# Optimization experiments

Hardware: AMD Instinct MI355X
Metric: run time of the kernel (lower is better)

The kernel has to match this reference:

```python
import jax, jax.numpy as jnp
import numpy as np

H, D, VD = 8, 64, 64
QD, KD, VDIM, OUT = 512, 512, 512, 512
N, QS, VS = 16, 512, 512
TEMP = 10.0              # softstair_temp
SCALING = D ** -0.5


def _softstair(x):
    fl = jnp.floor(x)
    return fl + jax.nn.sigmoid(TEMP * (jnp.abs(x - fl) - 0.5))


def setup_inputs() -> dict:
    key = jax.random.key(0)
    ks = jax.random.split(key, 24)
    f = jax.random.normal
    s = 0.03  # xavier-ish scale
    return {
        "Q": f(ks[0], (N, QS, QD), jnp.float32),
        "K": f(ks[1], (N, VS, KD), jnp.float32),
        "V": f(ks[2], (N, VS, VDIM), jnp.float32),
        "past_state": f(ks[3], (N, H, QS, D), jnp.float32),
        "past_attention": jax.random.uniform(ks[4], (N, H, QS, 1), jnp.float32),
        "value_positions": jnp.arange(VS, dtype=jnp.float32),
        "attention_mask": jnp.ones((N, QS, VS), jnp.int32),
        "Wq": f(ks[5], (QD, H * D), jnp.float32) * s,
        "Wk": f(ks[6], (KD, H * D), jnp.float32) * s,
        "Wv": f(ks[7], (VDIM, H * VD), jnp.float32) * s,
        "Wpos": f(ks[8], (QD, H * D), jnp.float32) * s,
        "bpos": f(ks[9], (H * D,), jnp.float32) * s,
        "Wsigma": f(ks[10], (H, D, 1), jnp.float32) * s,
        "Wrho": f(ks[11], (H, D, 3), jnp.float32) * s,
        "mix_w": f(ks[12], (QD, 1), jnp.float32) * s,
        "mix_b": f(ks[13], (1,), jnp.float32) * s,
        "gru_wi": f(ks[14], (D, 3 * D), jnp.float32) * s,
        "gru_wh": f(ks[15], (D, 3 * D), jnp.float32) * s,
        "gru_bi": f(ks[16], (3 * D,), jnp.float32) * s,
        "gru_bh": f(ks[17], (3 * D,), jnp.float32) * s,
        "Wc": f(ks[18], (H * VD, OUT), jnp.float32) * s,
    }


def reference(Q, K, V, past_state, past_attention, value_positions, attention_mask,
              Wq, Wk, Wv, Wpos, bpos, Wsigma, Wrho, mix_w, mix_b,
              gru_wi, gru_wh, gru_bi, gru_bh, Wc):
    n, qS, _ = Q.shape
    vS = K.shape[1]
    mask_f = attention_mask.astype(jnp.float32)          # [N,qS,vS]
    mask_b = attention_mask.astype(bool)[:, None]        # [N,1,qS,vS]
    lengths = jnp.sum(mask_f, axis=-1)                   # [N,qS]
    l_1 = jnp.maximum(1.0, lengths - 1.0)[:, None, :, None]
    step_size = 1.0 / l_1                                # [N,1,qS,1]
    nvp = value_positions[None, None, None, :] * step_size  # [N,1,qS,vS]

    # mix gate
    mix = jax.nn.sigmoid(Q @ mix_w + mix_b)[:, None]     # [N,1,qS,1]

    # projections -> [N,H,S,d]
    Qpos = (Q @ Wpos + bpos).reshape(n, qS, H, D).transpose(0, 2, 1, 3)
    Qh = (Q @ Wq).reshape(n, qS, H, D).transpose(0, 2, 1, 3)
    Kh = (K @ Wk).reshape(n, vS, H, D).transpose(0, 2, 1, 3)
    Vh = (V @ Wv).reshape(n, vS, H, VD).transpose(0, 2, 1, 3)

    # content attention
    content = jnp.einsum('bhqd,bhkd->bhqk', Qh, Kh) * SCALING
    content_attn = jax.nn.softmax(jnp.where(mask_b, content, -jnp.inf), axis=-1)

    # GRUCell update (torch gate order r,z,n) on relu(Qpos) with past_state
    x = jax.nn.relu(Qpos)
    gi = x @ gru_wi + gru_bi
    gh = past_state @ gru_wh + gru_bh
    ir, iz, inn = jnp.split(gi, 3, axis=-1)
    hr, hz, hn = jnp.split(gh, 3, axis=-1)
    r = jax.nn.sigmoid(ir + hr)
    z = jax.nn.sigmoid(iz + hz)
    nn_ = jnp.tanh(inn + r * hn)
    state = (1.0 - z) * nn_ + z * past_state             # [N,H,qS,D]

    # location (Gaussian) attention
    sigma = (jax.nn.relu(jnp.einsum('bhqd,hde->bhqe', state, Wsigma)) + 0.27) \
            / lengths[:, None, :, None]                  # [N,H,qS,1]
    rho = jnp.einsum('bhqd,hde->bhqe', state, Wrho)      # [N,H,qS,3]
    steps = _softstair(rho[..., 0:1])
    attn_gate = jax.nn.sigmoid(rho[..., 1:2])
    bias_gate = jax.nn.sigmoid(rho[..., 2:3])
    mu_ = steps * step_size + attn_gate * past_attention + bias_gate
    # leaky clamp to [0,1]
    mu = jnp.maximum(0.01 * mu_, jnp.minimum(mu_, 1.0 + 0.01 * mu_))
    diff = nvp - mu                                      # [N,H,qS,vS]
    gauss = jnp.exp(-(diff * diff) / (2.0 * sigma * sigma))
    g = gauss * mask_f[:, None]
    pos_attn = g / jnp.sum(g + 1e-20, axis=-1, keepdims=True)

    scores = mix * pos_attn + (1.0 - mix) * content_attn
    attended = jnp.einsum('bhqk,bhkv->bhqv', scores, Vh)
    out = attended.transpose(0, 2, 1, 3).reshape(n, qS, H * VD) @ Wc
    return out
```

## Files before the change

### kernel.cpp

```cpp
#include <hip/hip_runtime.h>


typedef __bf16 bf16;
typedef __bf16 bfx8 __attribute__((ext_vector_type(8)));
typedef float v4f __attribute__((ext_vector_type(4)));

__device__ inline float sigm(float x) { return 1.0f / (1.0f + expf(-x)); }

__device__ inline v4f mfma16(bfx8 a, bfx8 b, v4f c) {
    return __builtin_amdgcn_mfma_f32_16x16x32_bf16(a, b, c, 0, 0, 0);
}

__device__ inline void split8(const float* __restrict__ p, bfx8& hi, bfx8& lo) {
    float4 x = *(const float4*)p;
    float4 y = *(const float4*)(p + 4);
    float v[8] = {x.x, x.y, x.z, x.w, y.x, y.y, y.z, y.w};
#pragma unroll
    for (int j = 0; j < 8; ++j) {
        bf16 h = (bf16)v[j];
        hi[j] = h;
        lo[j] = (bf16)(v[j] - (float)h);
    }
}

__device__ inline unsigned short bfbits(float v) {
    bf16 h = (bf16)v;
    return __builtin_bit_cast(unsigned short, h);
}
__device__ inline float bffrom(unsigned short u) {
    return (float)__builtin_bit_cast(bf16, u);
}

__global__ __launch_bounds__(256) void conv_qkv_kernel(
    const float* __restrict__ s0, const float* __restrict__ s1, const float* __restrict__ s2,
    bf16* __restrict__ d0, bf16* __restrict__ d1, bf16* __restrict__ d2) {
    int tb = blockIdx.x >> 11;
    const float* src = tb == 0 ? s0 : (tb == 1 ? s1 : s2);
    bf16* dst = tb == 0 ? d0 : (tb == 1 ? d1 : d2);
    long i0 = (long)(blockIdx.x & 2047) * 2048 + threadIdx.x * 8;
    float4 x = *(const float4*)(src + i0);
    float4 y = *(const float4*)(src + i0 + 4);
    bfx8 o;
    o[0] = (bf16)x.x; o[1] = (bf16)x.y; o[2] = (bf16)x.z; o[3] = (bf16)x.w;
    o[4] = (bf16)y.x; o[5] = (bf16)y.y; o[6] = (bf16)y.z; o[7] = (bf16)y.w;
    *(bfx8*)(dst + i0) = o;
}

struct TW { const float* src[5]; bf16* dst[5]; bf16* dstlo[5]; };

__global__ __launch_bounds__(256) void trans_w_kernel(TW a) {
    __shared__ float tile[64][68];
    const float* src = a.src[blockIdx.y];
    bf16* dst = a.dst[blockIdx.y];
    bf16* dlo = a.dstlo[blockIdx.y];
    const int rbase = (blockIdx.x >> 3) * 64, cbase = (blockIdx.x & 7) * 64;
    const int t = threadIdx.x;
    const int r = t >> 2, cc = (t & 3) * 16;
    {
        const float* p = src + (long)(rbase + r) * 512 + cbase + cc;
        float4 x0 = *(const float4*)p, x1 = *(const float4*)(p + 4);
        float4 x2 = *(const float4*)(p + 8), x3 = *(const float4*)(p + 12);
        *(float4*)(&tile[r][cc]) = x0;
        *(float4*)(&tile[r][cc + 4]) = x1;
        *(float4*)(&tile[r][cc + 8]) = x2;
        *(float4*)(&tile[r][cc + 12]) = x3;
    }
    __syncthreads();
    {
        bfx8 h0, h1, l0, l1;
#pragma unroll
        for (int j = 0; j < 8; ++j) {
            float v0 = tile[cc + j][r];
            float v1 = tile[cc + 8 + j][r];
            bf16 a0 = (bf16)v0, a1 = (bf16)v1;
            h0[j] = a0; l0[j] = (bf16)(v0 - (float)a0);
            h1[j] = a1; l1[j] = (bf16)(v1 - (float)a1);
        }
        bf16* p = dst + (long)(cbase + r) * 512 + rbase + cc;
        *(bfx8*)p = h0;
        *(bfx8*)(p + 8) = h1;
        if (dlo) {
            bf16* pl = dlo + (long)(cbase + r) * 512 + rbase + cc;
            *(bfx8*)pl = l0;
            *(bfx8*)(pl + 8) = l1;
        }
    }
}

__global__ void gru_prep_kernel(const float* __restrict__ gwi, const float* __restrict__ gwh,
                                bf16* ih, bf16* il, bf16* hh, bf16* hl) {
    const float* src = blockIdx.x ? gwh : gwi;
    bf16* dh = blockIdx.x ? hh : ih;
    bf16* dl = blockIdx.x ? hl : il;
    int n = threadIdx.x;
    for (int k = 0; k < 64; ++k) {
        float v = src[k * 192 + n];
        bf16 h = (bf16)v;
        dh[n * 64 + k] = h;
        dl[n * 64 + k] = (bf16)(v - (float)h);
    }
}

template <bool TRANSC, typename OutT>
__global__ __launch_bounds__(256) void gemm_bt(
    const bf16* __restrict__ A, const bf16* __restrict__ BT,
    OutT* __restrict__ C) {
    __shared__ bf16 As[64][72];
    __shared__ bf16 Bs[64][72];

    const int mbase = blockIdx.x * 64, nbase = blockIdx.y * 64;
    const int t = threadIdx.x;
    const int wave = t >> 6, lane = t & 63;
    const int quad = lane >> 4, c = lane & 15;
    const int wrow = (wave >> 1) * 32, wcol = (wave & 1) * 32;

    const v4f zero4 = {0.f, 0.f, 0.f, 0.f};
    v4f acc[2][2];
    acc[0][0] = zero4; acc[0][1] = zero4; acc[1][0] = zero4; acc[1][1] = zero4;

    const int sr = t >> 2, sch = t & 3;

    for (int k0 = 0; k0 < 512; k0 += 32) {
        bfx8 va = *(const bfx8*)(A + (long)(mbase + sr) * 512 + k0 + sch * 8);
        bfx8 vb = *(const bfx8*)(BT + (long)(nbase + sr) * 512 + k0 + sch * 8);
        *(bfx8*)(&As[sr][sch * 8]) = va;
        *(bfx8*)(&Bs[sr][sch * 8]) = vb;
        __syncthreads();

        bfx8 a0 = *(const bfx8*)(&As[wrow + c][quad * 8]);
        bfx8 a1 = *(const bfx8*)(&As[wrow + 16 + c][quad * 8]);
        bfx8 b0 = *(const bfx8*)(&Bs[wcol + c][quad * 8]);
        bfx8 b1 = *(const bfx8*)(&Bs[wcol + 16 + c][quad * 8]);
        acc[0][0] = mfma16(a0, b0, acc[0][0]);
        acc[0][1] = mfma16(a0, b1, acc[0][1]);
        acc[1][0] = mfma16(a1, b0, acc[1][0]);
        acc[1][1] = mfma16(a1, b1, acc[1][1]);
        __syncthreads();
    }

    if (TRANSC) {
#pragma unroll
        for (int tm = 0; tm < 2; ++tm)
#pragma unroll
            for (int tn = 0; tn < 2; ++tn)
#pragma unroll
                for (int i = 0; i < 4; ++i) {
                    int rl = wrow + tm * 16 + quad * 4 + i;
                    int cl = wcol + tn * 16 + c;
                    As[cl][rl] = (bf16)acc[tm][tn][i];
                }
        __syncthreads();
        OutT* CT = C + ((long)(mbase >> 9)) * 262144 + (long)nbase * 512 + (mbase & 511);
        const int rr = t >> 2, kc = (t & 3) * 16;
        bfx8 o0, o1;
#pragma unroll
        for (int j = 0; j < 8; ++j) { o0[j] = As[rr][kc + j]; o1[j] = As[rr][kc + 8 + j]; }
        *(bfx8*)(CT + (long)rr * 512 + kc) = o0;
        *(bfx8*)(CT + (long)rr * 512 + kc + 8) = o1;
    } else {
#pragma unroll
        for (int tm = 0; tm < 2; ++tm)
#pragma unroll
            for (int tn = 0; tn < 2; ++tn)
#pragma unroll
                for (int i = 0; i < 4; ++i) {
                    int row = mbase + wrow + tm * 16 + quad * 4 + i;
                    int col = nbase + wcol + tn * 16 + c;
                    C[(long)row * 512 + col] = (OutT)acc[tm][tn][i];
                }
    }
}

__global__ __launch_bounds__(256) void gemm_split_hl(
    const float* __restrict__ A, const bf16* __restrict__ BTh,
    const bf16* __restrict__ BTl, const float* __restrict__ bias,
    bf16* __restrict__ Ch, bf16* __restrict__ Cl) {
    __shared__ bf16 Ah[64][72], Al[64][72];
    __shared__ bf16 Bh[64][72], Bl[64][72];

    const int mbase = blockIdx.x * 64, nbase = blockIdx.y * 64;
    const int t = threadIdx.x;
    const int wave = t >> 6, lane = t & 63;
    const int quad = lane >> 4, c = lane & 15;
    const int wrow = (wave >> 1) * 32, wcol = (wave & 1) * 32;

    const v4f zero4 = {0.f, 0.f, 0.f, 0.f};
    v4f acc[2][2];
    acc[0][0] = zero4; acc[0][1] = zero4; acc[1][0] = zero4; acc[1][1] = zero4;

    const int sr = t >> 2, sch = t & 3;

    for (int k0 = 0; k0 < 512; k0 += 32) {
        bfx8 h, l;
        split8(A + (long)(mbase + sr) * 512 + k0 + sch * 8, h, l);
        *(bfx8*)(&Ah[sr][sch * 8]) = h;
        *(bfx8*)(&Al[sr][sch * 8]) = l;
        *(bfx8*)(&Bh[sr][sch * 8]) = *(const bfx8*)(BTh + (long)(nbase + sr) * 512 + k0 + sch * 8);
        *(bfx8*)(&Bl[sr][sch * 8]) = *(const bfx8*)(BTl + (long)(nbase + sr) * 512 + k0 + sch * 8);
        __syncthreads();

        bfx8 ah0 = *(const bfx8*)(&Ah[wrow + c][quad * 8]);
        bfx8 ah1 = *(const bfx8*)(&Ah[wrow + 16 + c][quad * 8]);
        bfx8 al0 = *(const bfx8*)(&Al[wrow + c][quad * 8]);
        bfx8 al1 = *(const bfx8*)(&Al[wrow + 16 + c][quad * 8]);
        bfx8 bh0 = *(const bfx8*)(&Bh[wcol + c][quad * 8]);
        bfx8 bh1 = *(const bfx8*)(&Bh[wcol + 16 + c][quad * 8]);
        bfx8 bl0 = *(const bfx8*)(&Bl[wcol + c][quad * 8]);
        bfx8 bl1 = *(const bfx8*)(&Bl[wcol + 16 + c][quad * 8]);
        acc[0][0] = mfma16(ah0, bh0, acc[0][0]);
        acc[0][0] = mfma16(ah0, bl0, acc[0][0]);
        acc[0][0] = mfma16(al0, bh0, acc[0][0]);
        acc[0][1] = mfma16(ah0, bh1, acc[0][1]);
        acc[0][1] = mfma16(ah0, bl1, acc[0][1]);
        acc[0][1] = mfma16(al0, bh1, acc[0][1]);
        acc[1][0] = mfma16(ah1, bh0, acc[1][0]);
        acc[1][0] = mfma16(ah1, bl0, acc[1][0]);
        acc[1][0] = mfma16(al1, bh0, acc[1][0]);
        acc[1][1] = mfma16(ah1, bh1, acc[1][1]);
        acc[1][1] = mfma16(ah1, bl1, acc[1][1]);
        acc[1][1] = mfma16(al1, bh1, acc[1][1]);
        __syncthreads();
    }

#pragma unroll
    for (int tm = 0; tm < 2; ++tm)
#pragma unroll
        for (int tn = 0; tn < 2; ++tn)
#pragma unroll
            for (int i = 0; i < 4; ++i) {
                int row = mbase + wrow + tm * 16 + quad * 4 + i;
                int col = nbase + wcol + tn * 16 + c;
                float v = fmaxf(acc[tm][tn][i] + bias[col], 0.f);
                bf16 h = (bf16)v;
                Ch[(long)row * 512 + col] = h;
                Cl[(long)row * 512 + col] = (bf16)(v - (float)h);
            }
}

__global__ __launch_bounds__(256) void mix_len_kernel(
    const float* __restrict__ Q, const int* __restrict__ mask,
    const float* __restrict__ mix_w, const float* __restrict__ mix_b,
    float* __restrict__ mixv, float* __restrict__ stepv, float* __restrict__ lenv,
    unsigned* __restrict__ maskbits) {
    int row = blockIdx.x * 4 + (threadIdx.x >> 6);
    int lane = threadIdx.x & 63;
    float dot = 0.f, ms = 0.f;
    unsigned myw = 0;
#pragma unroll
    for (int j = 0; j < 8; ++j) {
        float qv = Q[(long)row * 512 + j * 64 + lane];
        float wv = mix_w[j * 64 + lane];
        dot += qv * wv;
        int mv = mask[(long)row * 512 + j * 64 + lane];
        unsigned long long b = __ballot(mv != 0);
        ms += (float)__popcll(b);
        if ((lane >> 1) == j) myw = (unsigned)(b >> ((lane & 1) * 32));
    }
#pragma unroll
    for (int o = 32; o > 0; o >>= 1) dot += __shfl_xor(dot, o);
    if (lane < 16) maskbits[(long)row * 16 + lane] = myw;
    if (lane == 0) {
        mixv[row] = sigm(dot + mix_b[0]);
        lenv[row] = ms;
        stepv[row] = 1.0f / fmaxf(1.0f, ms - 1.0f);
    }
}

__global__ __launch_bounds__(256) void gru_fused_kernel(
    const bf16* __restrict__ Xh, const bf16* __restrict__ Xl,
    const float* __restrict__ hp,
    const bf16* __restrict__ wih, const bf16* __restrict__ wil,
    const bf16* __restrict__ whh, const bf16* __restrict__ whl,
    const float* __restrict__ gbi, const float* __restrict__ gbh,
    const float* __restrict__ pa, const float* __restrict__ Wsigma,
    const float* __restrict__ Wrho,
    const float* __restrict__ lenv, const float* __restrict__ stepv,
    float* __restrict__ muv, float* __restrict__ sigv) {
    __shared__ bf16 Wh[192][72], Wl[192][72];
    __shared__ float biL[384];

    const int b = blockIdx.x;
    const int qb = b & 7, nh = b >> 3, hd = nh & 7, n = nh >> 3;
    const int t = threadIdx.x;
    const int w = t >> 6, lane = t & 63, quad = lane >> 4, c = lane & 15;
    const int q0 = qb * 64 + w * 16;

    if (t < 192) { biL[t] = gbi[t]; biL[192 + t] = gbh[t]; }
#pragma unroll
    for (int it = 0; it < 6; ++it) {
        int task = it * 256 + t;
        int r = task >> 3, ch = task & 7;
        *(bfx8*)(&Wh[r][ch * 8]) = *(const bfx8*)(wih + r * 64 + ch * 8);
        *(bfx8*)(&Wl[r][ch * 8]) = *(const bfx8*)(wil + r * 64 + ch * 8);
    }
    __syncthreads();

    const v4f zero4 = {0.f, 0.f, 0.f, 0.f};
    v4f gi[12], gh[12];
#pragma unroll
    for (int nt = 0; nt < 12; ++nt) gi[nt] = zero4;
#pragma unroll
    for (int ks = 0; ks < 2; ++ks) {
        long ao = (long)(n * 512 + q0 + c) * 512 + hd * 64 + ks * 32 + quad * 8;
        bfx8 xh = *(const bfx8*)(Xh + ao);
        bfx8 xl = *(const bfx8*)(Xl + ao);
#pragma unroll
        for (int nt = 0; nt < 12; ++nt) {
            bfx8 bh = *(const bfx8*)(&Wh[nt * 16 + c][ks * 32 + quad * 8]);
            bfx8 bl = *(const bfx8*)(&Wl[nt * 16 + c][ks * 32 + quad * 8]);
            gi[nt] = mfma16(xh, bh, gi[nt]);
            gi[nt] = mfma16(xh, bl, gi[nt]);
            gi[nt] = mfma16(xl, bh, gi[nt]);
        }
    }
    __syncthreads();
#pragma unroll
    for (int it = 0; it < 6; ++it) {
        int task = it * 256 + t;
        int r = task >> 3, ch = task & 7;
        *(bfx8*)(&Wh[r][ch * 8]) = *(const bfx8*)(whh + r * 64 + ch * 8);
        *(bfx8*)(&Wl[r][ch * 8]) = *(const bfx8*)(whl + r * 64 + ch * 8);
    }
    __syncthreads();
#pragma unroll
    for (int nt = 0; nt < 12; ++nt) gh[nt] = zero4;
#pragma unroll
    for (int ks = 0; ks < 2; ++ks) {
        bfx8 ah, al;
        split8(hp + (long)(nh * 512 + q0 + c) * 64 + ks * 32 + quad * 8, ah, al);
#pragma unroll
        for (int nt = 0; nt < 12; ++nt) {
            bfx8 bh = *(const bfx8*)(&Wh[nt * 16 + c][ks * 32 + quad * 8]);
            bfx8 bl = *(const bfx8*)(&Wl[nt * 16 + c][ks * 32 + quad * 8]);
            gh[nt] = mfma16(ah, bh, gh[nt]);
            gh[nt] = mfma16(ah, bl, gh[nt]);
            gh[nt] = mfma16(al, bh, gh[nt]);
        }
    }

    float st[4][4];
#pragma unroll
    for (int t4 = 0; t4 < 4; ++t4) {
        float bir = biL[t4 * 16 + c];
        float biz = biL[64 + t4 * 16 + c];
        float bin = biL[128 + t4 * 16 + c];
        float bhr = biL[192 + t4 * 16 + c];
        float bhz = biL[256 + t4 * 16 + c];
        float bhn = biL[320 + t4 * 16 + c];
#pragma unroll
        for (int i = 0; i < 4; ++i) {
            int row = q0 + quad * 4 + i;
            float r = sigm(gi[t4][i] + bir + gh[t4][i] + bhr);
            float z = sigm(gi[t4 + 4][i] + biz + gh[t4 + 4][i] + bhz);
            float nn_ = tanhf(gi[t4 + 8][i] + bin + r * (gh[t4 + 8][i] + bhn));
            float hpv = hp[(long)(nh * 512 + row) * 64 + t4 * 16 + c];
            st[t4][i] = (1.0f - z) * nn_ + z * hpv;
        }
    }

    float ws_[4], wr0[4], wr1[4], wr2[4];
#pragma unroll
    for (int t4 = 0; t4 < 4; ++t4) {
        int d = t4 * 16 + c;
        ws_[t4] = Wsigma[hd * 64 + d];
        wr0[t4] = Wrho[(hd * 64 + d) * 3 + 0];
        wr1[t4] = Wrho[(hd * 64 + d) * 3 + 1];
        wr2[t4] = Wrho[(hd * 64 + d) * 3 + 2];
    }
#pragma unroll
    for (int i = 0; i < 4; ++i) {
        float s0 = 0.f, s1 = 0.f, s2 = 0.f, s3 = 0.f;
#pragma unroll
        for (int t4 = 0; t4 < 4; ++t4) {
            float sv = st[t4][i];
            s0 += sv * ws_[t4];
            s1 += sv * wr0[t4];
            s2 += sv * wr1[t4];
            s3 += sv * wr2[t4];
        }
#pragma unroll
        for (int o = 1; o < 16; o <<= 1) {
            s0 += __shfl_xor(s0, o);
            s1 += __shfl_xor(s1, o);
            s2 += __shfl_xor(s2, o);
            s3 += __shfl_xor(s3, o);
        }
        if (c == 0) {
            int row = q0 + quad * 4 + i;
            int idx = nh * 512 + row, rq = n * 512 + row;
            float L = lenv[rq], sp = stepv[rq];
            float sg = (fmaxf(s0, 0.f) + 0.27f) / L;
            float fl = floorf(s1);
            float steps = fl + sigm(10.0f * (fabsf(s1 - fl) - 0.5f));
            float ag = sigm(s2), bg = sigm(s3);
            float mu_ = steps * sp + ag * pa[idx] + bg;
            float mu = fmaxf(0.01f * mu_, fminf(mu_, 1.0f + 0.01f * mu_));
            muv[idx] = mu;
            sigv[idx] = sg;
        }
    }
}

__global__ __launch_bounds__(256) void attn_fused_kernel(
    const bf16* __restrict__ Qh, const bf16* __restrict__ Kh,
    const bf16* __restrict__ VhT, const unsigned* __restrict__ maskbits,
    const float* __restrict__ vpos, const float* __restrict__ mixv,
    const float* __restrict__ stepv, const float* __restrict__ muv,
    const float* __restrict__ sigv, bf16* __restrict__ att) {
    __shared__ alignas(16) char KVraw[128 * 72 * 2];
    __shared__ bf16 Qs[16][72];
    __shared__ bf16 Plds[16][520];
    __shared__ float vps[512];
    __shared__ float rmax[4][16], rsum[4][16], rgsum[4][16];
    __shared__ float rowmu[16], rowsig[16], rowstep[16], rowmix[16];
    bf16 (*Ks)[72] = (bf16(*)[72])KVraw;
    bf16 (*Vs)[136] = (bf16(*)[136])KVraw;

    const int b = blockIdx.x;
    const int qt = b & 31, nh = b >> 5, hd = nh & 7, n = nh >> 3;
    const int t = threadIdx.x;

    if (t < 16) {
        int q = qt * 16 + t;
        int idx = nh * 512 + q, rq = n * 512 + q;
        rowmu[t] = muv[idx];
        rowsig[t] = sigv[idx];
        rowstep[t] = stepv[rq];
        rowmix[t] = mixv[rq];
    }
    vps[t] = vpos[t];
    vps[256 + t] = vpos[256 + t];
    if (t < 128) {
        int r = t >> 3, ch = t & 7;
        bfx8 v = *(const bfx8*)(Qh + (long)(n * 512 + qt * 16 + r) * 512 + hd * 64 + ch * 8);
        *(bfx8*)(&Qs[r][ch * 8]) = v;
    }
    __syncthreads();

    const int wave = t >> 6, lane = t & 63;
    const int quad = lane >> 4, c = lane & 15;
    const int qloc = quad * 4;

    bfx8 afr0 = *(const bfx8*)(&Qs[c][quad * 8]);
    bfx8 afr1 = *(const bfx8*)(&Qs[c][32 + quad * 8]);

    const v4f zero4 = {0.f, 0.f, 0.f, 0.f};
    v4f acc[8];
#pragma unroll
    for (int i = 0; i < 8; ++i) acc[i] = zero4;

#pragma unroll
    for (int ph = 0; ph < 4; ++ph) {
#pragma unroll
        for (int it = 0; it < 4; ++it) {
            int task = it * 256 + t;
            int r = task >> 3, ch = task & 7;
            *(bfx8*)(&Ks[r][ch * 8]) =
                *(const bfx8*)(Kh + (long)(n * 512 + ph * 128 + r) * 512 + hd * 64 + ch * 8);
        }
        __syncthreads();
#pragma unroll
        for (int tt = 0; tt < 2; ++tt) {
            int t8 = ph * 2 + tt;
            int kr = wave * 32 + tt * 16 + c;
            bfx8 b0 = *(const bfx8*)(&Ks[kr][quad * 8]);
            bfx8 b1 = *(const bfx8*)(&Ks[kr][32 + quad * 8]);
            acc[t8] = mfma16(afr0, b0, acc[t8]);
            acc[t8] = mfma16(afr1, b1, acc[t8]);
        }
        __syncthreads();
    }

#pragma unroll
    for (int t8 = 0; t8 < 8; ++t8) acc[t8] = acc[t8] * 0.125f;

    unsigned mw[4][4];
#pragma unroll
    for (int i = 0; i < 4; ++i) {
        const unsigned* mrow = maskbits + (long)(n * 512 + qt * 16 + qloc + i) * 16 + wave;
        mw[i][0] = mrow[0];
        mw[i][1] = mrow[4];
        mw[i][2] = mrow[8];
        mw[i][3] = mrow[12];
    }

#pragma unroll
    for (int i = 0; i < 4; ++i) {
        float mx = -3.0e38f;
#pragma unroll
        for (int t8 = 0; t8 < 8; ++t8)
            if ((mw[i][t8 >> 1] >> ((t8 & 1) * 16 + c)) & 1) mx = fmaxf(mx, acc[t8][i]);
        mx = fmaxf(mx, __shfl_xor(mx, 1));
        mx = fmaxf(mx, __shfl_xor(mx, 2));
        mx = fmaxf(mx, __shfl_xor(mx, 4));
        mx = fmaxf(mx, __shfl_xor(mx, 8));
        if (c == 0) rmax[wave][qloc + i] = mx;
    }
    __syncthreads();

    float gmx[4], inv2s[4];
#pragma unroll
    for (int i = 0; i < 4; ++i) {
        gmx[i] = fmaxf(fmaxf(rmax[0][qloc + i], rmax[1][qloc + i]),
                       fmaxf(rmax[2][qloc + i], rmax[3][qloc + i]));
        float sg = rowsig[qloc + i];
        inv2s[i] = 0.5f / (sg * sg);
    }

    float psum[4] = {0.f, 0.f, 0.f, 0.f};
    float gsum[4] = {0.f, 0.f, 0.f, 0.f};
    unsigned pg[8][4];
#pragma unroll
    for (int t8 = 0; t8 < 8; ++t8) {
        int k = (t8 >> 1) * 128 + wave * 32 + (t8 & 1) * 16 + c;
        float vp = vps[k];
#pragma unroll
        for (int i = 0; i < 4; ++i) {
            int on = (mw[i][t8 >> 1] >> ((t8 & 1) * 16 + c)) & 1;
            float pv = on ? expf(acc[t8][i] - gmx[i]) : 0.f;
            float d = vp * rowstep[qloc + i] - rowmu[qloc + i];
            float gv = on ? expf(-(d * d) * inv2s[i]) : 0.f;
            psum[i] += pv;
            gsum[i] += gv;
            pg[t8][i] = ((unsigned)bfbits(gv) << 16) | (unsigned)bfbits(pv);
        }
    }
#pragma unroll
    for (int i = 0; i < 4; ++i) {
#pragma unroll
        for (int o = 1; o < 16; o <<= 1) {
            psum[i] += __shfl_xor(psum[i], o);
            gsum[i] += __shfl_xor(gsum[i], o);
        }
        if (c == 0) {
            rsum[wave][qloc + i] = psum[i];
            rgsum[wave][qloc + i] = gsum[i];
        }
    }
    __syncthreads();

    float ac[4], bc[4];
#pragma unroll
    for (int i = 0; i < 4; ++i) {
        float Sp = rsum[0][qloc + i] + rsum[1][qloc + i] + rsum[2][qloc + i] + rsum[3][qloc + i];
        float Sg = rgsum[0][qloc + i] + rgsum[1][qloc + i] + rgsum[2][qloc + i] +
                   rgsum[3][qloc + i] + 512.0f * 1e-20f;
        float m_ = rowmix[qloc + i];
        ac[i] = (1.0f - m_) / Sp;
        bc[i] = m_ / Sg;
    }

#pragma unroll
    for (int t8 = 0; t8 < 8; ++t8) {
        int k = (t8 >> 1) * 128 + wave * 32 + (t8 & 1) * 16 + c;
#pragma unroll
        for (int i = 0; i < 4; ++i) {
            float pv = bffrom((unsigned short)(pg[t8][i] & 0xffffu));
            float gv = bffrom((unsigned short)(pg[t8][i] >> 16));
            Plds[qloc + i][k] = (bf16)(pv * ac[i] + gv * bc[i]);
        }
    }
    __syncthreads();

    v4f accO = zero4;
#pragma unroll
    for (int ph = 0; ph < 4; ++ph) {
#pragma unroll
        for (int it = 0; it < 4; ++it) {
            int task = it * 256 + t;
            int v = task >> 4, ch = task & 15;
            *(bfx8*)(&Vs[v][ch * 8]) =
                *(const bfx8*)(VhT + (long)(n * 512 + hd * 64 + v) * 512 + ph * 128 + ch * 8);
        }
        __syncthreads();
#pragma unroll
        for (int ks = 0; ks < 4; ++ks) {
            bfx8 af = *(const bfx8*)(&Plds[c][ph * 128 + ks * 32 + quad * 8]);
            bfx8 bf_ = *(const bfx8*)(&Vs[wave * 16 + c][ks * 32 + quad * 8]);
            accO = mfma16(af, bf_, accO);
        }
        __syncthreads();
    }

#pragma unroll
    for (int i = 0; i < 4; ++i) {
        att[(long)(n * 512 + qt * 16 + quad * 4 + i) * 512 + hd * 64 + wave * 16 + c] =
            (bf16)accO[i];
    }
}

extern "C" void kernel_launch(void* const* d_in, const int* in_sizes, int n_in,
                              void* d_out, int out_size, void* d_ws, size_t ws_size,
                              hipStream_t stream) {
    (void)in_sizes; (void)n_in; (void)out_size; (void)ws_size;

    const float* Q = (const float*)d_in[0];
    const float* K = (const float*)d_in[1];
    const float* V = (const float*)d_in[2];
    const float* past_state = (const float*)d_in[3];
    const float* past_att = (const float*)d_in[4];
    const float* vpos = (const float*)d_in[5];
    const int* mask = (const int*)d_in[6];
    const float* Wq = (const float*)d_in[7];
    const float* Wk = (const float*)d_in[8];
    const float* Wv = (const float*)d_in[9];
    const float* Wpos = (const float*)d_in[10];
    const float* bpos = (const float*)d_in[11];
    const float* Wsigma = (const float*)d_in[12];
    const float* Wrho = (const float*)d_in[13];
    const float* mix_w = (const float*)d_in[14];
    const float* mix_b = (const float*)d_in[15];
    const float* gwi = (const float*)d_in[16];
    const float* gwh = (const float*)d_in[17];
    const float* gbi = (const float*)d_in[18];
    const float* gbh = (const float*)d_in[19];
    const float* Wc = (const float*)d_in[20];
    float* out = (float*)d_out;

    char* p = (char*)d_ws;
    const size_t SZB = 8192UL * 512 * 2;
    const size_t SZW = 512UL * 512 * 2;
    bf16* Qc = (bf16*)p;    p += SZB;
    bf16* Kc = (bf16*)p;    p += SZB;
    bf16* Vc = (bf16*)p;    p += SZB;
    bf16* WqT = (bf16*)p;   p += SZW;
    bf16* WkT = (bf16*)p;   p += SZW;
    bf16* WvT = (bf16*)p;   p += SZW;
    bf16* WpT = (bf16*)p;   p += SZW;
    bf16* WpTl = (bf16*)p;  p += SZW;
    bf16* WcT = (bf16*)p;   p += SZW;
    bf16* wih = (bf16*)p;   p += 24576;
    bf16* wil = (bf16*)p;   p += 24576;
    bf16* whh = (bf16*)p;   p += 24576;
    bf16* whl = (bf16*)p;   p += 24576;
    bf16* Qh = (bf16*)p;    p += SZB;
    bf16* Kh = (bf16*)p;    p += SZB;
    bf16* VhT = (bf16*)p;   p += SZB;
    bf16* Xh = (bf16*)p;
    bf16* att = Xh;         p += SZB;
    bf16* Xl = (bf16*)p;    p += SZB;
    unsigned* maskbits = (unsigned*)p;   p += 8192UL * 16 * 4;
    float* mixv = (float*)p;  p += 32768;
    float* stepv = (float*)p; p += 32768;
    float* lenv = (float*)p;  p += 32768;
    float* muv = (float*)p;   p += 262144;
    float* sigv = (float*)p;  p += 262144;

    dim3 blk(256);
    dim3 gProj(128, 8, 1);

    conv_qkv_kernel<<<dim3(6144), blk, 0, stream>>>(Q, K, V, Qc, Kc, Vc);

    TW tw;
    tw.src[0] = Wq; tw.src[1] = Wk; tw.src[2] = Wv; tw.src[3] = Wpos; tw.src[4] = Wc;
    tw.dst[0] = WqT; tw.dst[1] = WkT; tw.dst[2] = WvT; tw.dst[3] = WpT; tw.dst[4] = WcT;
    tw.dstlo[0] = nullptr; tw.dstlo[1] = nullptr; tw.dstlo[2] = nullptr;
    tw.dstlo[3] = WpTl; tw.dstlo[4] = nullptr;
    trans_w_kernel<<<dim3(64, 5), blk, 0, stream>>>(tw);

    gru_prep_kernel<<<dim3(2), dim3(192), 0, stream>>>(gwi, gwh, wih, wil, whh, whl);

    gemm_bt<false, bf16><<<gProj, blk, 0, stream>>>(Qc, WqT, Qh);
    gemm_bt<false, bf16><<<gProj, blk, 0, stream>>>(Kc, WkT, Kh);
    gemm_bt<true, bf16><<<gProj, blk, 0, stream>>>(Vc, WvT, VhT);
    gemm_split_hl<<<gProj, blk, 0, stream>>>(Q, WpT, WpTl, bpos, Xh, Xl);

    mix_len_kernel<<<dim3(2048), blk, 0, stream>>>(Q, mask, mix_w, mix_b, mixv, stepv, lenv, maskbits);

    gru_fused_kernel<<<dim3(1024), blk, 0, stream>>>(
        Xh, Xl, past_state, wih, wil, whh, whl, gbi, gbh, past_att, Wsigma, Wrho,
        lenv, stepv, muv, sigv);

    attn_fused_kernel<<<dim3(4096), blk, 0, stream>>>(
        Qh, Kh, VhT, maskbits, vpos, mixv, stepv, muv, sigv, att);

    gemm_bt<false, float><<<gProj, blk, 0, stream>>>(att, WcT, out);
}
```

Baseline: 385.2 us.

## Load attention operands directly from global, recompute exps, batch QKV GEMMs

The attention kernel no longer stages Q, K and V through shared memory. MFMA fragments are read straight from global memory, which removes the per-phase barriers, and the key ordering per wave is changed to match. Mask bits are staged once in shared memory and repacked per thread. The packed bf16 P/G values are no longer kept in registers and the exponentials are recomputed with fast __expf, trading extra math for lower register pressure. The three projection GEMMs are merged into one launch over blockIdx.z. The direct global reads rely on L2/cache reuse across waves, and __expf may lose a little precision.

```diff
diff --git a/kernel.cpp b/kernel.cpp
--- a/kernel.cpp
+++ b/kernel.cpp
@@ -5,7 +5,7 @@
 typedef __bf16 bfx8 __attribute__((ext_vector_type(8)));
 typedef float v4f __attribute__((ext_vector_type(4)));
 
-__device__ inline float sigm(float x) { return 1.0f / (1.0f + expf(-x)); }
+__device__ inline float sigm(float x) { return 1.0f / (1.0f + __expf(-x)); }
 
 __device__ inline v4f mfma16(bfx8 a, bfx8 b, v4f c) {
     return __builtin_amdgcn_mfma_f32_16x16x32_bf16(a, b, c, 0, 0, 0);
@@ -21,14 +21,6 @@
         hi[j] = h;
         lo[j] = (bf16)(v[j] - (float)h);
     }
-}
-
-__device__ inline unsigned short bfbits(float v) {
-    bf16 h = (bf16)v;
-    return __builtin_bit_cast(unsigned short, h);
-}
-__device__ inline float bffrom(unsigned short u) {
-    return (float)__builtin_bit_cast(bf16, u);
 }
 
 __global__ __launch_bounds__(256) void conv_qkv_kernel(
@@ -58,12 +50,10 @@
     const int r = t >> 2, cc = (t & 3) * 16;
     {
         const float* p = src + (long)(rbase + r) * 512 + cbase + cc;
-        float4 x0 = *(const float4*)p, x1 = *(const float4*)(p + 4);
-        float4 x2 = *(const float4*)(p + 8), x3 = *(const float4*)(p + 12);
-        *(float4*)(&tile[r][cc]) = x0;
-        *(float4*)(&tile[r][cc + 4]) = x1;
-        *(float4*)(&tile[r][cc + 8]) = x2;
-        *(float4*)(&tile[r][cc + 12]) = x3;
+        *(float4*)(&tile[r][cc]) = *(const float4*)p;
+        *(float4*)(&tile[r][cc + 4]) = *(const float4*)(p + 4);
+        *(float4*)(&tile[r][cc + 8]) = *(const float4*)(p + 8);
+        *(float4*)(&tile[r][cc + 12]) = *(const float4*)(p + 12);
     }
     __syncthreads();
     {
@@ -101,12 +91,16 @@
     }
 }
 
-template <bool TRANSC, typename OutT>
-__global__ __launch_bounds__(256) void gemm_bt(
-    const bf16* __restrict__ A, const bf16* __restrict__ BT,
-    OutT* __restrict__ C) {
+struct G3 { const bf16* A[3]; const bf16* BT[3]; bf16* C[3]; };
+
+__global__ __launch_bounds__(256) void gemm_bt3(G3 g) {
     __shared__ bf16 As[64][72];
     __shared__ bf16 Bs[64][72];
+
+    const int z = blockIdx.z;
+    const bf16* __restrict__ A = g.A[z];
+    const bf16* __restrict__ BT = g.BT[z];
+    bf16* __restrict__ C = g.C[z];
 
     const int mbase = blockIdx.x * 64, nbase = blockIdx.y * 64;
     const int t = threadIdx.x;
@@ -138,7 +132,7 @@
         __syncthreads();
     }
 
-    if (TRANSC) {
+    if (z == 2) {
 #pragma unroll
         for (int tm = 0; tm < 2; ++tm)
 #pragma unroll
@@ -150,7 +144,7 @@
                     As[cl][rl] = (bf16)acc[tm][tn][i];
                 }
         __syncthreads();
-        OutT* CT = C + ((long)(mbase >> 9)) * 262144 + (long)nbase * 512 + (mbase & 511);
+        bf16* CT = C + ((long)(mbase >> 9)) * 262144 + (long)nbase * 512 + (mbase & 511);
         const int rr = t >> 2, kc = (t & 3) * 16;
         bfx8 o0, o1;
 #pragma unroll
@@ -166,9 +160,56 @@
                 for (int i = 0; i < 4; ++i) {
                     int row = mbase + wrow + tm * 16 + quad * 4 + i;
                     int col = nbase + wcol + tn * 16 + c;
-                    C[(long)row * 512 + col] = (OutT)acc[tm][tn][i];
+                    C[(long)row * 512 + col] = (bf16)acc[tm][tn][i];
                 }
     }
+}
+
+__global__ __launch_bounds__(256) void gemm_out(
+    const bf16* __restrict__ A, const bf16* __restrict__ BT, float* __restrict__ C) {
+    __shared__ bf16 As[64][72];
+    __shared__ bf16 Bs[64][72];
+
+    const int mbase = blockIdx.x * 64, nbase = blockIdx.y * 64;
+    const int t = threadIdx.x;
+    const int wave = t >> 6, lane = t & 63;
+    const int quad = lane >> 4, c = lane & 15;
+    const int wrow = (wave >> 1) * 32, wcol = (wave & 1) * 32;
+
+    const v4f zero4 = {0.f, 0.f, 0.f, 0.f};
+    v4f acc[2][2];
+    acc[0][0] = zero4; acc[0][1] = zero4; acc[1][0] = zero4; acc[1][1] = zero4;
+
+    const int sr = t >> 2, sch = t & 3;
+
+    for (int k0 = 0; k0 < 512; k0 += 32) {
+        bfx8 va = *(const bfx8*)(A + (long)(mbase + sr) * 512 + k0 + sch * 8);
+        bfx8 vb = *(const bfx8*)(BT + (long)(nbase + sr) * 512 + k0 + sch * 8);
+        *(bfx8*)(&As[sr][sch * 8]) = va;
+        *(bfx8*)(&Bs[sr][sch * 8]) = vb;
+        __syncthreads();
+
+        bfx8 a0 = *(const bfx8*)(&As[wrow + c][quad * 8]);
+        bfx8 a1 = *(const bfx8*)(&As[wrow + 16 + c][quad * 8]);
+        bfx8 b0 = *(const bfx8*)(&Bs[wcol + c][quad * 8]);
+        bfx8 b1 = *(const bfx8*)(&Bs[wcol + 16 + c][quad * 8]);
+        acc[0][0] = mfma16(a0, b0, acc[0][0]);
+        acc[0][1] = mfma16(a0, b1, acc[0][1]);
+        acc[1][0] = mfma16(a1, b0, acc[1][0]);
+        acc[1][1] = mfma16(a1, b1, acc[1][1]);
+        __syncthreads();
+    }
+
+#pragma unroll
+    for (int tm = 0; tm < 2; ++tm)
+#pragma unroll
+        for (int tn = 0; tn < 2; ++tn)
+#pragma unroll
+            for (int i = 0; i < 4; ++i) {
+                int row = mbase + wrow + tm * 16 + quad * 4 + i;
+                int col = nbase + wcol + tn * 16 + c;
+                C[(long)row * 512 + col] = acc[tm][tn][i];
+            }
 }
 
 __global__ __launch_bounds__(256) void gemm_split_hl(
@@ -407,14 +448,11 @@
     const float* __restrict__ vpos, const float* __restrict__ mixv,
     const float* __restrict__ stepv, const float* __restrict__ muv,
     const float* __restrict__ sigv, bf16* __restrict__ att) {
-    __shared__ alignas(16) char KVraw[128 * 72 * 2];
-    __shared__ bf16 Qs[16][72];
     __shared__ bf16 Plds[16][520];
     __shared__ float vps[512];
+    __shared__ unsigned mb[16][16];
     __shared__ float rmax[4][16], rsum[4][16], rgsum[4][16];
     __shared__ float rowmu[16], rowsig[16], rowstep[16], rowmix[16];
-    bf16 (*Ks)[72] = (bf16(*)[72])KVraw;
-    bf16 (*Vs)[136] = (bf16(*)[136])KVraw;
 
     const int b = blockIdx.x;
     const int qt = b & 31, nh = b >> 5, hd = nh & 7, n = nh >> 3;
@@ -430,58 +468,42 @@
     }
     vps[t] = vpos[t];
     vps[256 + t] = vpos[256 + t];
-    if (t < 128) {
-        int r = t >> 3, ch = t & 7;
-        bfx8 v = *(const bfx8*)(Qh + (long)(n * 512 + qt * 16 + r) * 512 + hd * 64 + ch * 8);
-        *(bfx8*)(&Qs[r][ch * 8]) = v;
-    }
-    __syncthreads();
+    mb[t >> 4][t & 15] = maskbits[(long)(n * 512 + qt * 16 + (t >> 4)) * 16 + (t & 15)];
 
     const int wave = t >> 6, lane = t & 63;
     const int quad = lane >> 4, c = lane & 15;
     const int qloc = quad * 4;
 
-    bfx8 afr0 = *(const bfx8*)(&Qs[c][quad * 8]);
-    bfx8 afr1 = *(const bfx8*)(&Qs[c][32 + quad * 8]);
+    const bf16* qrow = Qh + (long)(n * 512 + qt * 16 + c) * 512 + hd * 64 + quad * 8;
+    bfx8 afr0 = *(const bfx8*)qrow;
+    bfx8 afr1 = *(const bfx8*)(qrow + 32);
 
     const v4f zero4 = {0.f, 0.f, 0.f, 0.f};
     v4f acc[8];
 #pragma unroll
     for (int i = 0; i < 8; ++i) acc[i] = zero4;
 
-#pragma unroll
-    for (int ph = 0; ph < 4; ++ph) {
-#pragma unroll
-        for (int it = 0; it < 4; ++it) {
-            int task = it * 256 + t;
-            int r = task >> 3, ch = task & 7;
-            *(bfx8*)(&Ks[r][ch * 8]) =
-                *(const bfx8*)(Kh + (long)(n * 512 + ph * 128 + r) * 512 + hd * 64 + ch * 8);
-        }
-        __syncthreads();
-#pragma unroll
-        for (int tt = 0; tt < 2; ++tt) {
-            int t8 = ph * 2 + tt;
-            int kr = wave * 32 + tt * 16 + c;
-            bfx8 b0 = *(const bfx8*)(&Ks[kr][quad * 8]);
-            bfx8 b1 = *(const bfx8*)(&Ks[kr][32 + quad * 8]);
-            acc[t8] = mfma16(afr0, b0, acc[t8]);
-            acc[t8] = mfma16(afr1, b1, acc[t8]);
-        }
-        __syncthreads();
-    }
-
+    const bf16* kbase = Kh + (long)(n * 512 + wave * 128 + c) * 512 + hd * 64 + quad * 8;
+#pragma unroll
+    for (int t8 = 0; t8 < 8; ++t8) {
+        bfx8 b0 = *(const bfx8*)(kbase + (long)t8 * 16 * 512);
+        bfx8 b1 = *(const bfx8*)(kbase + (long)t8 * 16 * 512 + 32);
+        acc[t8] = mfma16(afr0, b0, acc[t8]);
+        acc[t8] = mfma16(afr1, b1, acc[t8]);
+    }
 #pragma unroll
     for (int t8 = 0; t8 < 8; ++t8) acc[t8] = acc[t8] * 0.125f;
 
-    unsigned mw[4][4];
-#pragma unroll
-    for (int i = 0; i < 4; ++i) {
-        const unsigned* mrow = maskbits + (long)(n * 512 + qt * 16 + qloc + i) * 16 + wave;
-        mw[i][0] = mrow[0];
-        mw[i][1] = mrow[4];
-        mw[i][2] = mrow[8];
-        mw[i][3] = mrow[12];
+    __syncthreads();
+
+    unsigned mbits[4] = {0u, 0u, 0u, 0u};
+#pragma unroll
+    for (int t8 = 0; t8 < 8; ++t8) {
+        int wd = wave * 4 + (t8 >> 1);
+        int bit = (t8 & 1) * 16 + c;
+#pragma unroll
+        for (int i = 0; i < 4; ++i)
+            mbits[i] |= ((mb[qloc + i][wd] >> bit) & 1u) << t8;
     }
 
 #pragma unroll
@@ -489,7 +511,7 @@
         float mx = -3.0e38f;
 #pragma unroll
         for (int t8 = 0; t8 < 8; ++t8)
-            if ((mw[i][t8 >> 1] >> ((t8 & 1) * 16 + c)) & 1) mx = fmaxf(mx, acc[t8][i]);
+            if ((mbits[i] >> t8) & 1u) mx = fmaxf(mx, acc[t8][i]);
         mx = fmaxf(mx, __shfl_xor(mx, 1));
         mx = fmaxf(mx, __shfl_xor(mx, 2));
         mx = fmaxf(mx, __shfl_xor(mx, 4));
@@ -509,20 +531,18 @@
 
     float psum[4] = {0.f, 0.f, 0.f, 0.f};
     float gsum[4] = {0.f, 0.f, 0.f, 0.f};
-    unsigned pg[8][4];
 #pragma unroll
     for (int t8 = 0; t8 < 8; ++t8) {
-        int k = (t8 >> 1) * 128 + wave * 32 + (t8 & 1) * 16 + c;
+        int k = wave * 128 + t8 * 16 + c;
         float vp = vps[k];
 #pragma unroll
         for (int i = 0; i < 4; ++i) {
-            int on = (mw[i][t8 >> 1] >> ((t8 & 1) * 16 + c)) & 1;
-            float pv = on ? expf(acc[t8][i] - gmx[i]) : 0.f;
+            int on = (mbits[i] >> t8) & 1;
+            float pv = on ? __expf(acc[t8][i] - gmx[i]) : 0.f;
             float d = vp * rowstep[qloc + i] - rowmu[qloc + i];
-            float gv = on ? expf(-(d * d) * inv2s[i]) : 0.f;
+            float gv = on ? __expf(-(d * d) * inv2s[i]) : 0.f;
             psum[i] += pv;
             gsum[i] += gv;
-            pg[t8][i] = ((unsigned)bfbits(gv) << 16) | (unsigned)bfbits(pv);
         }
     }
 #pragma unroll
@@ -552,34 +572,26 @@
 
 #pragma unroll
     for (int t8 = 0; t8 < 8; ++t8) {
-        int k = (t8 >> 1) * 128 + wave * 32 + (t8 & 1) * 16 + c;
+        int k = wave * 128 + t8 * 16 + c;
+        float vp = vps[k];
 #pragma unroll
         for (int i = 0; i < 4; ++i) {
-            float pv = bffrom((unsigned short)(pg[t8][i] & 0xffffu));
-            float gv = bffrom((unsigned short)(pg[t8][i] >> 16));
+            int on = (mbits[i] >> t8) & 1;
+            float pv = on ? __expf(acc[t8][i] - gmx[i]) : 0.f;
+            float d = vp * rowstep[qloc + i] - rowmu[qloc + i];
+            float gv = on ? __expf(-(d * d) * inv2s[i]) : 0.f;
             Plds[qloc + i][k] = (bf16)(pv * ac[i] + gv * bc[i]);
         }
     }
     __syncthreads();
 
     v4f accO = zero4;
-#pragma unroll
-    for (int ph = 0; ph < 4; ++ph) {
-#pragma unroll
-        for (int it = 0; it < 4; ++it) {
-            int task = it * 256 + t;
-            int v = task >> 4, ch = task & 15;
-            *(bfx8*)(&Vs[v][ch * 8]) =
-                *(const bfx8*)(VhT + (long)(n * 512 + hd * 64 + v) * 512 + ph * 128 + ch * 8);
-        }
-        __syncthreads();
-#pragma unroll
-        for (int ks = 0; ks < 4; ++ks) {
-            bfx8 af = *(const bfx8*)(&Plds[c][ph * 128 + ks * 32 + quad * 8]);
-            bfx8 bf_ = *(const bfx8*)(&Vs[wave * 16 + c][ks * 32 + quad * 8]);
-            accO = mfma16(af, bf_, accO);
-        }
-        __syncthreads();
+    const bf16* vrow = VhT + (long)(n * 512 + hd * 64 + wave * 16 + c) * 512 + quad * 8;
+#pragma unroll
+    for (int ks = 0; ks < 16; ++ks) {
+        bfx8 af = *(const bfx8*)(&Plds[c][ks * 32 + quad * 8]);
+        bfx8 bf_ = *(const bfx8*)(vrow + ks * 32);
+        accO = mfma16(af, bf_, accO);
     }
 
 #pragma unroll
@@ -660,9 +672,12 @@
 
     gru_prep_kernel<<<dim3(2), dim3(192), 0, stream>>>(gwi, gwh, wih, wil, whh, whl);
 
-    gemm_bt<false, bf16><<<gProj, blk, 0, stream>>>(Qc, WqT, Qh);
-    gemm_bt<false, bf16><<<gProj, blk, 0, stream>>>(Kc, WkT, Kh);
-    gemm_bt<true, bf16><<<gProj, blk, 0, stream>>>(Vc, WvT, VhT);
+    G3 g;
+    g.A[0] = Qc; g.A[1] = Kc; g.A[2] = Vc;
+    g.BT[0] = WqT; g.BT[1] = WkT; g.BT[2] = WvT;
+    g.C[0] = Qh; g.C[1] = Kh; g.C[2] = VhT;
+    gemm_bt3<<<dim3(128, 8, 3), blk, 0, stream>>>(g);
+
     gemm_split_hl<<<gProj, blk, 0, stream>>>(Q, WpT, WpTl, bpos, Xh, Xl);
 
     mix_len_kernel<<<dim3(2048), blk, 0, stream>>>(Q, mask, mix_w, mix_b, mixv, stepv, lenv, maskbits);
@@ -674,5 +689,5 @@
     attn_fused_kernel<<<dim3(4096), blk, 0, stream>>>(
         Qh, Kh, VhT, maskbits, vpos, mixv, stepv, muv, sigv, att);
 
-    gemm_bt<false, float><<<gProj, blk, 0, stream>>>(att, WcT, out);
-}
+    gemm_out<<<gProj, blk, 0, stream>>>(att, WcT, out);
+}
```

Result: faster. 365.9 us (-5.0%).
